# Kernel optimization log

Hardware: AMD Instinct MI355X
Metric: run time of the kernel (lower is better)

The kernel has to match this reference:

```python
import jax, jax.numpy as jnp
import numpy as np

B, S, IN, OUT = 4, 2048, 4096, 11008

def setup_inputs() -> dict:
    key = jax.random.key(0)
    k1, k2, k3, k4, k5 = jax.random.split(key, 5)
    x = jax.random.normal(k1, (B, S, IN), dtype=jnp.float32)
    weight_4bit = jax.random.randint(k2, (OUT, IN), 0, 16, dtype=jnp.int32)
    # per-tensor scalar scale / zero_point, stored with shape [1] like the torch buffers
    scale = jax.random.uniform(k3, (1,), dtype=jnp.float32, minval=0.001, maxval=0.01)
    zero_point = jnp.round(jax.random.uniform(k4, (1,), dtype=jnp.float32, minval=0.0, maxval=15.0))
    bias = jax.random.normal(k5, (OUT,), dtype=jnp.float32) * 0.01
    return {"x": x, "weight_4bit": weight_4bit, "scale": scale, "zero_point": zero_point, "bias": bias}

def reference(x, weight_4bit, scale, zero_point, bias):
    # dequantize: w_rec = (w_q - zero_point) * scale, shape [OUT, IN]
    w = (weight_4bit.astype(jnp.float32) - zero_point) * scale
    # out[b,s,o] = sum_i x[b,s,i] * w[o,i] + bias[o]
    out = jnp.einsum('bsi,oi->bso', x, w) + bias
    return out
```

## Files before the change

### kernel.cpp

```cpp
#include <hip/hip_runtime.h>
#include <cstdint>
#include <cstddef>

#define Mdim 8192
#define Ndim 11008
#define Kdim 4096
#define BM 128
#define BN 128
#define BK 64

typedef __attribute__((ext_vector_type(8))) __bf16 bf16x8;
typedef __attribute__((ext_vector_type(4))) float floatx4;

__device__ inline unsigned short f2bf(float f) {
    union { float f; unsigned u; } v; v.f = f;
    unsigned r = v.u + 0x7fffu + ((v.u >> 16) & 1u);
    return (unsigned short)(r >> 16);
}

__global__ void cvt_x_kernel(const float4* __restrict__ x, ushort4* __restrict__ o, int n4) {
    int i = blockIdx.x * blockDim.x + threadIdx.x;
    if (i >= n4) return;
    float4 v = x[i];
    ushort4 r;
    r.x = f2bf(v.x); r.y = f2bf(v.y); r.z = f2bf(v.z); r.w = f2bf(v.w);
    o[i] = r;
}

__global__ void cvt_w_kernel(const int4* __restrict__ w, ushort4* __restrict__ o,
                             const float* __restrict__ scale, const float* __restrict__ zp,
                             int n4) {
    int i = blockIdx.x * blockDim.x + threadIdx.x;
    if (i >= n4) return;
    float s = scale[0];
    float z = zp[0];
    int4 q = w[i];
    ushort4 r;
    r.x = f2bf(((float)q.x - z) * s);
    r.y = f2bf(((float)q.y - z) * s);
    r.z = f2bf(((float)q.z - z) * s);
    r.w = f2bf(((float)q.w - z) * s);
    o[i] = r;
}

__global__ __launch_bounds__(256) void gemm_kernel(const short* __restrict__ A,
                                                   const short* __restrict__ B,
                                                   const float* __restrict__ bias,
                                                   float* __restrict__ C) {
    __shared__ __align__(16) short As[BM * BK];
    __shared__ __align__(16) short Bs[BN * BK];

    const int tid  = threadIdx.x;
    const int lane = tid & 63;
    const int wave = tid >> 6;
    const int waveM = wave >> 1;
    const int waveN = wave & 1;
    const int l15  = lane & 15;
    const int quad = lane >> 4;

    const int mBase = blockIdx.y * BM;
    const int nBase = blockIdx.x * BN;

    floatx4 acc[4][4];
    #pragma unroll
    for (int i = 0; i < 4; ++i)
        #pragma unroll
        for (int j = 0; j < 4; ++j)
            acc[i][j] = (floatx4)0.0f;

    const short* ga[4];
    const short* gb[4];
    int ldsoff[4];
    #pragma unroll
    for (int r = 0; r < 4; ++r) {
        int li  = r * 256 + tid;
        int row = li >> 3;
        int pc  = li & 7;
        int gc  = pc ^ (row & 7);
        ga[r] = A + (size_t)(mBase + row) * Kdim + gc * 8;
        gb[r] = B + (size_t)(nBase + row) * Kdim + gc * 8;
        ldsoff[r] = li * 8;
    }

    for (int k0 = 0; k0 < Kdim; k0 += BK) {
        #pragma unroll
        for (int r = 0; r < 4; ++r)
            __builtin_amdgcn_global_load_lds(
                (const __attribute__((address_space(1))) void*)(ga[r] + k0),
                (__attribute__((address_space(3))) void*)(As + ldsoff[r]), 16, 0, 0);
        #pragma unroll
        for (int r = 0; r < 4; ++r)
            __builtin_amdgcn_global_load_lds(
                (const __attribute__((address_space(1))) void*)(gb[r] + k0),
                (__attribute__((address_space(3))) void*)(Bs + ldsoff[r]), 16, 0, 0);
        __syncthreads();

        #pragma unroll
        for (int kk = 0; kk < 2; ++kk) {
            bf16x8 af[4], bfr[4];
            const int c = kk * 4 + quad;
            #pragma unroll
            for (int i = 0; i < 4; ++i) {
                int rowA = waveM * 64 + i * 16 + l15;
                af[i]  = *(const bf16x8*)(As + (rowA * 8 + (c ^ (rowA & 7))) * 8);
                int rowB = waveN * 64 + i * 16 + l15;
                bfr[i] = *(const bf16x8*)(Bs + (rowB * 8 + (c ^ (rowB & 7))) * 8);
            }
            #pragma unroll
            for (int i = 0; i < 4; ++i)
                #pragma unroll
                for (int j = 0; j < 4; ++j)
                    acc[i][j] = __builtin_amdgcn_mfma_f32_16x16x32_bf16(
                        af[i], bfr[j], acc[i][j], 0, 0, 0);
        }
        __syncthreads();
    }

    #pragma unroll
    for (int j = 0; j < 4; ++j) {
        int col = nBase + waveN * 64 + j * 16 + l15;
        float bv = bias[col];
        #pragma unroll
        for (int i = 0; i < 4; ++i) {
            int row0 = mBase + waveM * 64 + i * 16 + quad * 4;
            #pragma unroll
            for (int r = 0; r < 4; ++r)
                C[(size_t)(row0 + r) * Ndim + col] = acc[i][j][r] + bv;
        }
    }
}

extern "C" void kernel_launch(void* const* d_in, const int* in_sizes, int n_in,
                              void* d_out, int out_size, void* d_ws, size_t ws_size,
                              hipStream_t stream) {
    const float* x     = (const float*)d_in[0];
    const int*   w4    = (const int*)  d_in[1];
    const float* scale = (const float*)d_in[2];
    const float* zp    = (const float*)d_in[3];
    const float* bias  = (const float*)d_in[4];
    float* out = (float*)d_out;

    short* Abf = (short*)d_ws;
    short* Wbf = Abf + (size_t)Mdim * Kdim;

    const int nx4 = Mdim * Kdim / 4;
    cvt_x_kernel<<<nx4 / 256, 256, 0, stream>>>((const float4*)x, (ushort4*)Abf, nx4);

    const int nw4 = Ndim * Kdim / 4;
    cvt_w_kernel<<<nw4 / 256, 256, 0, stream>>>((const int4*)w4, (ushort4*)Wbf, scale, zp, nw4);

    dim3 grid(Ndim / BN, Mdim / BM);
    gemm_kernel<<<grid, 256, 0, stream>>>(Abf, Wbf, bias, out);
}
```

Measured before the change: 1.450 ms.

## Group-M tile swizzle for GEMM and widen bf16 conversion stores to 16 bytes

The GEMM now uses a 1D grid whose block index is remapped so that groups of 16 M-tiles sweep the N dimension together. Concurrently running blocks then share A and B tiles, which should improve L2 and MALL reuse. The two conversion kernels each process 8 elements per thread and write packed uint4 (16-byte) stores instead of 8-byte ushort4 stores, cutting the number of store instructions. The tile mapping relies on the M tile count (64) dividing evenly by GROUP_M.

Result: faster. 1.284 ms (-11.4%).

```diff
diff --git a/kernel.cpp b/kernel.cpp
--- a/kernel.cpp
+++ b/kernel.cpp
@@ -8,38 +8,47 @@
 #define BM 128
 #define BN 128
 #define BK 64
+#define GROUP_M 16
 
 typedef __attribute__((ext_vector_type(8))) __bf16 bf16x8;
 typedef __attribute__((ext_vector_type(4))) float floatx4;
 
-__device__ inline unsigned short f2bf(float f) {
+__device__ inline unsigned f2bf(float f) {
     union { float f; unsigned u; } v; v.f = f;
     unsigned r = v.u + 0x7fffu + ((v.u >> 16) & 1u);
-    return (unsigned short)(r >> 16);
+    return r >> 16;
+}
+__device__ inline unsigned pack2(float lo, float hi) {
+    return f2bf(lo) | (f2bf(hi) << 16);
 }
 
-__global__ void cvt_x_kernel(const float4* __restrict__ x, ushort4* __restrict__ o, int n4) {
+__global__ void cvt_x_kernel(const float4* __restrict__ x, uint4* __restrict__ o, int n8) {
     int i = blockIdx.x * blockDim.x + threadIdx.x;
-    if (i >= n4) return;
-    float4 v = x[i];
-    ushort4 r;
-    r.x = f2bf(v.x); r.y = f2bf(v.y); r.z = f2bf(v.z); r.w = f2bf(v.w);
+    if (i >= n8) return;
+    float4 a = x[2 * i];
+    float4 b = x[2 * i + 1];
+    uint4 r;
+    r.x = pack2(a.x, a.y);
+    r.y = pack2(a.z, a.w);
+    r.z = pack2(b.x, b.y);
+    r.w = pack2(b.z, b.w);
     o[i] = r;
 }
 
-__global__ void cvt_w_kernel(const int4* __restrict__ w, ushort4* __restrict__ o,
+__global__ void cvt_w_kernel(const int4* __restrict__ w, uint4* __restrict__ o,
                              const float* __restrict__ scale, const float* __restrict__ zp,
-                             int n4) {
+                             int n8) {
     int i = blockIdx.x * blockDim.x + threadIdx.x;
-    if (i >= n4) return;
+    if (i >= n8) return;
     float s = scale[0];
     float z = zp[0];
-    int4 q = w[i];
-    ushort4 r;
-    r.x = f2bf(((float)q.x - z) * s);
-    r.y = f2bf(((float)q.y - z) * s);
-    r.z = f2bf(((float)q.z - z) * s);
-    r.w = f2bf(((float)q.w - z) * s);
+    int4 a = w[2 * i];
+    int4 b = w[2 * i + 1];
+    uint4 r;
+    r.x = pack2(((float)a.x - z) * s, ((float)a.y - z) * s);
+    r.y = pack2(((float)a.z - z) * s, ((float)a.w - z) * s);
+    r.z = pack2(((float)b.x - z) * s, ((float)b.y - z) * s);
+    r.w = pack2(((float)b.z - z) * s, ((float)b.w - z) * s);
     o[i] = r;
 }
 
@@ -58,8 +67,14 @@
     const int l15  = lane & 15;
     const int quad = lane >> 4;
 
-    const int mBase = blockIdx.y * BM;
-    const int nBase = blockIdx.x * BN;
+    const int NT = Ndim / BN;
+    int pid   = blockIdx.x;
+    int group = pid / (GROUP_M * NT);
+    int rem   = pid % (GROUP_M * NT);
+    int mt    = group * GROUP_M + (rem % GROUP_M);
+    int nt    = rem / GROUP_M;
+    const int mBase = mt * BM;
+    const int nBase = nt * BN;
 
     floatx4 acc[4][4];
     #pragma unroll
@@ -143,12 +158,12 @@
     short* Abf = (short*)d_ws;
     short* Wbf = Abf + (size_t)Mdim * Kdim;
 
-    const int nx4 = Mdim * Kdim / 4;
-    cvt_x_kernel<<<nx4 / 256, 256, 0, stream>>>((const float4*)x, (ushort4*)Abf, nx4);
+    const int nx8 = Mdim * Kdim / 8;
+    cvt_x_kernel<<<nx8 / 256, 256, 0, stream>>>((const float4*)x, (uint4*)Abf, nx8);
 
-    const int nw4 = Ndim * Kdim / 4;
-    cvt_w_kernel<<<nw4 / 256, 256, 0, stream>>>((const int4*)w4, (ushort4*)Wbf, scale, zp, nw4);
+    const int nw8 = Ndim * Kdim / 8;
+    cvt_w_kernel<<<nw8 / 256, 256, 0, stream>>>((const int4*)w4, (uint4*)Wbf, scale, zp, nw8);
 
-    dim3 grid(Ndim / BN, Mdim / BM);
-    gemm_kernel<<<grid, 256, 0, stream>>>(Abf, Wbf, bias, out);
+    const int nblocks = (Ndim / BN) * (Mdim / BM);
+    gemm_kernel<<<nblocks, 256, 0, stream>>>(Abf, Wbf, bias, out);
 }
```
